# Performance work log

Measured on AMD Instinct MI355X. Metric: run time of the kernel, lower is better.

Reference implementation:

```python
import jax, jax.numpy as jnp
import numpy as np

DIM = 256
HEADS = 8
HD = DIM // HEADS          # 32
WS = 8                     # window size
TOPK = 4
SCALE = HD ** -0.5


def setup_inputs() -> dict:
    key = jax.random.key(0)
    k1, k2, k3 = jax.random.split(key, 3)
    B, H, W = 8, 64, 64
    x = jax.random.normal(k1, (B, DIM, H, W), dtype=jnp.float32)
    # 1x1 conv weights (BN folded -> weight + bias), fan-in scaled to keep logits sane
    w_qkv = jax.random.normal(k2, (3 * DIM, DIM), dtype=jnp.float32) / np.sqrt(DIM)
    b_qkv = jnp.zeros((3 * DIM,), dtype=jnp.float32)
    w_proj = jax.random.normal(k3, (DIM, DIM), dtype=jnp.float32) / np.sqrt(DIM)
    b_proj = jnp.zeros((DIM,), dtype=jnp.float32)
    return {"x": x, "w_qkv": w_qkv, "b_qkv": b_qkv, "w_proj": w_proj, "b_proj": b_proj}


def _window_partition(t, ws):
    # t: [BH, D, H, W] -> [BH, R, ws*ws, D]
    bh, d, h, w = t.shape
    gh, gw = h // ws, w // ws
    t = t.reshape(bh, d, gh, ws, gw, ws)
    t = t.transpose(0, 2, 4, 3, 5, 1)          # [BH, gh, gw, ws, ws, D]
    return t.reshape(bh, gh * gw, ws * ws, d)


def reference(x, w_qkv, b_qkv, w_proj, b_proj):
    B, C, H, W = x.shape
    gh, gw = H // WS, W // WS
    R, T = gh * gw, WS * WS
    BH = B * HEADS

    # qkv 1x1 conv
    qkv = jnp.einsum('bchw,oc->bohw', x, w_qkv) + b_qkv[None, :, None, None]
    q, k, v = jnp.split(qkv, 3, axis=1)                       # each [B, C, H, W]

    def to_bh(t):
        return t.reshape(BH, HD, H, W)

    q_w = _window_partition(to_bh(q), WS)                     # [BH, R, T, HD]
    k_w = _window_partition(to_bh(k), WS)
    v_w = _window_partition(to_bh(v), WS)

    # region-level routing: mean-pooled region tokens
    q_r = q_w.mean(axis=2)                                    # [BH, R, HD]
    k_r = k_w.mean(axis=2)
    attn_r = jnp.einsum('brd,bkd->brk', q_r, k_r) * SCALE     # [BH, R, R]
    topk = min(TOPK, R)
    _, topk_idx = jax.lax.top_k(attn_r, topk)                 # [BH, R, K]

    # gather top-k key/value windows per query region
    bidx = jnp.arange(BH)[:, None, None]
    k_sel = k_w[bidx, topk_idx]                               # [BH, R, K, T, HD]
    v_sel = v_w[bidx, topk_idx]
    k_sel = k_sel.reshape(BH, R, topk * T, HD)
    v_sel = v_sel.reshape(BH, R, topk * T, HD)

    # token-level attention inside routed regions
    attn = jnp.einsum('brtd,brsd->brts', q_w, k_sel) * SCALE  # [BH, R, T, K*T]
    attn = jax.nn.softmax(attn, axis=-1)
    out_w = jnp.einsum('brts,brsd->brtd', attn, v_sel)        # [BH, R, T, HD]

    # window reverse -> [BH, HD, H, W]
    out = out_w.reshape(BH, gh, gw, WS, WS, HD)
    out = out.transpose(0, 5, 1, 3, 2, 4).reshape(BH, HD, H, W)
    out = out.reshape(B, C, H, W)

    out = jnp.einsum('bchw,oc->bohw', out, w_proj) + b_proj[None, :, None, None]
    return out
```

## Files before the change

### kernel.cpp

```cpp
#include <hip/hip_runtime.h>
#include <hip/hip_bf16.h>

#define ATT_SCALE 0.17677669529663687f
#define EXP_C1 0.2550349235534668f
#define EXP_C2 23.083120654223400f

typedef short v8s __attribute__((ext_vector_type(8)));
typedef float v4f __attribute__((ext_vector_type(4)));
typedef float v16f __attribute__((ext_vector_type(16)));
typedef const __attribute__((address_space(1))) unsigned int gu32;
typedef __attribute__((address_space(3))) unsigned int lu32;

__device__ __forceinline__ void g2l16(const void* g, void* l) {
  __builtin_amdgcn_global_load_lds((gu32*)g, (lu32*)l, 16, 0, 0);
}

__device__ __forceinline__ float bflo(unsigned u){ union{unsigned i;float f;}x; x.i=u<<16; return x.f; }
__device__ __forceinline__ float bfhi(unsigned u){ union{unsigned i;float f;}x; x.i=u&0xffff0000u; return x.f; }
__device__ __forceinline__ unsigned short bf16r(float v){
  __hip_bfloat16 h = __float2bfloat16(v);
  return *reinterpret_cast<unsigned short*>(&h);
}
__device__ __forceinline__ unsigned pack_bf2(float a, float b){
  return (unsigned)bf16r(a) | ((unsigned)bf16r(b) << 16);
}
__device__ __forceinline__ unsigned cvtpk(float lo, float hi){
  unsigned r;
  asm("v_cvt_pk_bf16_f32 %0, %1, %2" : "=v"(r) : "v"(lo), "v"(hi));
  return r;
}
__device__ __forceinline__ void pl32swap(unsigned &a, unsigned &b){
  asm volatile("v_permlane32_swap_b32 %0, %1" : "+v"(a), "+v"(b));
}

__global__ __launch_bounds__(256) void k_prep(const float* __restrict__ x,
                                              const float* __restrict__ w_qkv,
                                              const float* __restrict__ w_proj,
                                              unsigned short* __restrict__ Xb,
                                              unsigned short* __restrict__ Wq,
                                              unsigned short* __restrict__ Wp,
                                              float* __restrict__ part) {
  __shared__ __align__(16) char hbuf[8192];
  __shared__ float pbuf[512];
  const int blk = blockIdx.x;
  const int t = threadIdx.x;
  if (blk >= 2048) {
    const int m = blk - 2048;
    const float* src = (m < 768) ? (w_qkv + m*256) : (w_proj + (size_t)(m - 768)*256);
    unsigned short* dst = (m < 768) ? (Wq + m*256) : (Wp + (size_t)(m - 768)*256);
    dst[t] = bf16r(src[t]);
    return;
  }
  const int b = blk >> 8, cc = (blk >> 6) & 3, pc = blk & 63;
  const int c0 = cc << 6, p0 = pc << 6;
  const int wv = t >> 6, lane = t & 63;

  float hi[16];
  const float* xp = x + ((size_t)(b*256 + c0 + wv*16))*4096 + p0 + lane;
  #pragma unroll
  for (int i = 0; i < 16; ++i) hi[i] = xp[(size_t)i*4096];

  #pragma unroll
  for (int i = 0; i < 16; ++i) {
    float s = hi[i];
    s += __shfl_xor(s, 1);
    s += __shfl_xor(s, 2);
    s += __shfl_xor(s, 4);
    if ((lane & 7) == 0) pbuf[(wv*16 + i)*8 + (lane >> 3)] = s;
  }

  #pragma unroll
  for (int gi = 0; gi < 2; ++gi) {
    uint4 uh;
    uh.x = pack_bf2(hi[gi*8+0], hi[gi*8+1]); uh.y = pack_bf2(hi[gi*8+2], hi[gi*8+3]);
    uh.z = pack_bf2(hi[gi*8+4], hi[gi*8+5]); uh.w = pack_bf2(hi[gi*8+6], hi[gi*8+7]);
    int off = lane*128 + ((wv*32 + gi*16) ^ ((lane & 7) << 4));
    *(uint4*)(hbuf + off) = uh;
  }
  __syncthreads();
  const size_t rowbase = ((size_t)(b*4096 + p0)) * 512 + (size_t)c0*2;
  #pragma unroll
  for (int s = 0; s < 2; ++s) {
    int gidx = s*256 + t;
    int row = gidx >> 3, gb = (gidx & 7) << 4;
    uint4 vh = *(const uint4*)(hbuf + row*128 + gb);
    *(uint4*)((char*)Xb + rowbase + (size_t)row*512 + gb) = vh;
  }
  const size_t pbase = ((size_t)(b*64 + pc)*256 + c0)*8;
  part[pbase + t]       = pbuf[t];
  part[pbase + 256 + t] = pbuf[t + 256];
}

__global__ __launch_bounds__(256) void k_xmr(const float* __restrict__ part,
                                             float* __restrict__ xmean) {
  const int blk = blockIdx.x;
  const int item = blk & 7;
  const int b = blk >> 6, rh = (blk >> 3) & 7;
  const int t = threadIdx.x;
  const int flat = item*256 + t;
  float acc = 0.f;
  const float* pp = part + (size_t)(b*64 + rh*8)*2048 + flat;
  #pragma unroll
  for (int j = 0; j < 8; ++j) acc += pp[(size_t)j*2048];
  const int c = flat >> 3, wc = flat & 7;
  xmean[(size_t)((b*256 + c) << 6) + (rh << 3) + wc] = acc * 0.015625f;
}

__global__ __launch_bounds__(256) void k_route(const float* __restrict__ xmean,
                                               const float* __restrict__ w_qkv,
                                               const float* __restrict__ b_qkv,
                                               int* __restrict__ topk) {
  __shared__ float xm[128][64];
  __shared__ float qr[64][33];
  __shared__ float kr[64][33];
  const int bh = blockIdx.x, b = bh >> 3, head = bh & 7;
  const int tid = threadIdx.x;
  const int d = tid & 31, r0 = tid >> 5;
  float qacc[8], kacc[8];
  const float bq = b_qkv[head*32 + d], bk = b_qkv[256 + head*32 + d];
  #pragma unroll
  for (int i = 0; i < 8; ++i) { qacc[i] = bq; kacc[i] = bk; }

  for (int c0 = 0; c0 < 256; c0 += 128) {
    __syncthreads();
    #pragma unroll
    for (int i = 0; i < 32; ++i) {
      int idx = i*256 + tid;
      int row = idx >> 6, col = idx & 63;
      xm[row][col] = xmean[(size_t)(b*256 + c0 + row)*64 + col];
    }
    __syncthreads();
    const float* wqp = w_qkv + (head*32 + d)*256 + c0;
    const float* wkp = w_qkv + (256 + head*32 + d)*256 + c0;
    for (int c = 0; c < 128; ++c) {
      float wq = wqp[c], wk = wkp[c];
      #pragma unroll
      for (int i = 0; i < 8; ++i) {
        float xv = xm[c][r0 + 8*i];
        qacc[i] += wq * xv;
        kacc[i] += wk * xv;
      }
    }
  }
  #pragma unroll
  for (int i = 0; i < 8; ++i) { qr[r0+8*i][d] = qacc[i]; kr[r0+8*i][d] = kacc[i]; }
  __syncthreads();

  float* ar = &xm[0][0];
  for (int item = tid; item < 4096; item += 256) {
    int i = item >> 6, j = item & 63;
    float s = 0.f;
    #pragma unroll
    for (int dd = 0; dd < 32; ++dd) s += qr[i][dd]*kr[j][dd];
    ar[i*64 + j] = s;
  }
  __syncthreads();
  if (tid < 64) {
    for (int kk = 0; kk < 4; ++kk) {
      float best = -3e38f; int bj = 0;
      for (int j = 0; j < 64; ++j) {
        float v = ar[tid*64 + j];
        if (v > best) { best = v; bj = j; }
      }
      ar[tid*64 + bj] = -3e38f;
      topk[(bh*64 + tid)*4 + kk] = bj;
    }
  }
}

template<int EPI>
__global__ __launch_bounds__(256) void k_gemm(
    const unsigned short* __restrict__ Wstk,
    const unsigned short* __restrict__ Bmat,
    const float* __restrict__ bias,
    unsigned short* __restrict__ qbuf, unsigned short* __restrict__ kbuf,
    unsigned short* __restrict__ vbuf, float* __restrict__ outp) {
  __shared__ __align__(16) char lds[32768];
  const int tid = threadIdx.x;
  const int wv = tid >> 6, lane = tid & 63;
  const int nt = blockIdx.x, mt = blockIdx.y;

  const char* xsrc = (const char*)Bmat
      + (size_t)(nt*64 + (lane >> 5))*512 + (lane & 31)*16;
  #pragma unroll
  for (int o = 0; o < 8; ++o) {
    int op = wv*8 + o;
    g2l16(xsrc + (size_t)(op*2)*512, lds + op*1024);
  }

  const char* wrowbase = (const char*)Wstk
      + ((size_t)(mt*128 + wv*32 + (lane & 15)))*512 + ((lane >> 4) << 4);
  v8s a[4][2][2];
  #pragma unroll
  for (int kt = 0; kt < 4; ++kt)
    #pragma unroll
    for (int kk = 0; kk < 2; ++kk)
      #pragma unroll
      for (int i = 0; i < 2; ++i)
        a[kt][kk][i] = *(const v8s*)(wrowbase + (size_t)(i*16)*512 + kt*128 + kk*64);

  v4f acc[2][4];
  #pragma unroll
  for (int i = 0; i < 2; ++i)
    #pragma unroll
    for (int j = 0; j < 4; ++j) acc[i][j] = (v4f){0.f,0.f,0.f,0.f};

  asm volatile("s_waitcnt vmcnt(0)" ::: "memory");
  __syncthreads();

  #pragma unroll
  for (int kt = 0; kt < 4; ++kt) {
    #pragma unroll
    for (int kk = 0; kk < 2; ++kk) {
      const int kb = kk*64 + ((lane>>4)<<4);
      v8s b[4];
      #pragma unroll
      for (int j = 0; j < 4; ++j) {
        int nr = j*16 + (lane & 15);
        b[j] = *(const v8s*)(lds + nr*512 + kt*128 + (kb ^ ((nr & 7) << 4)));
      }
      #pragma unroll
      for (int i = 0; i < 2; ++i)
        #pragma unroll
        for (int j = 0; j < 4; ++j)
          acc[i][j] = __builtin_amdgcn_mfma_f32_16x16x32_bf16(a[kt][kk][i], b[j], acc[i][j], 0, 0, 0);
    }
  }

  if (EPI == 0) {
    if (mt < 4) {
      unsigned short* outbuf = (mt < 2) ? qbuf : kbuf;
      #pragma unroll
      for (int i = 0; i < 2; ++i) {
        int o = mt*128 + wv*32 + i*16 + ((lane >> 4) << 2);
        int head = (o >> 5) & 7, d0 = o & 31;
        float b0 = bias[o], b1 = bias[o+1], b2 = bias[o+2], b3 = bias[o+3];
        #pragma unroll
        for (int j = 0; j < 4; ++j) {
          int p = nt*64 + j*16 + (lane & 15);
          int bb = p >> 12, ploc = p & 4095;
          int h = ploc >> 6, w = ploc & 63;
          int rr = ((h >> 3) << 3) | (w >> 3), tt = ((h & 7) << 3) | (w & 7);
          int bh = bb*8 + head;
          uint2 u;
          u.x = pack_bf2(acc[i][j][0] + b0, acc[i][j][1] + b1);
          u.y = pack_bf2(acc[i][j][2] + b2, acc[i][j][3] + b3);
          *(uint2*)(outbuf + (size_t)(((bh << 6) | rr)*64 + tt)*32 + d0) = u;
        }
      }
    } else {
      #pragma unroll
      for (int i = 0; i < 2; ++i) {
        int o = mt*128 + wv*32 + i*16 + ((lane >> 4) << 2);
        int vch = o - 512;
        int head = vch >> 5, d0 = vch & 31;
        float bv[4] = {bias[o], bias[o+1], bias[o+2], bias[o+3]};
        #pragma unroll
        for (int j = 0; j < 4; ++j) {
          int p = nt*64 + j*16 + (lane & 15);
          int bb = p >> 12, ploc = p & 4095;
          int h = ploc >> 6, w = ploc & 63;
          int rr = ((h >> 3) << 3) | (w >> 3), tt = ((h & 7) << 3) | (w & 7);
          int bh = bb*8 + head;
          size_t base = ((size_t)((bh << 6) | rr)*32 + d0)*64 + tt;
          #pragma unroll
          for (int c = 0; c < 4; ++c)
            vbuf[base + (size_t)c*64] = bf16r(acc[i][j][c] + bv[c]);
        }
      }
    }
  } else {
    #pragma unroll
    for (int i = 0; i < 2; ++i) {
      int o = mt*128 + wv*32 + i*16 + ((lane >> 4) << 2);
      float b0 = bias[o], b1 = bias[o+1], b2 = bias[o+2], b3 = bias[o+3];
      #pragma unroll
      for (int j = 0; j < 4; ++j) {
        int p = nt*64 + j*16 + (lane & 15);
        int bb = p >> 12, ploc = p & 4095;
        float* dst = outp + ((size_t)(bb*256 + o))*4096 + ploc;
        dst[0]     = acc[i][j][0] + b0;
        dst[4096]  = acc[i][j][1] + b1;
        dst[8192]  = acc[i][j][2] + b2;
        dst[12288] = acc[i][j][3] + b3;
      }
    }
  }
}

__global__ __launch_bounds__(256) void k_attn(const unsigned short* __restrict__ qw,
                                              const unsigned short* __restrict__ kw,
                                              const unsigned short* __restrict__ vwt,
                                              const int* __restrict__ topk,
                                              unsigned short* __restrict__ owt) {
  const int lane = threadIdx.x & 63;
  const int W = blockIdx.x*4 + (threadIdx.x >> 6);
  const int bh = W >> 6, rr = W & 63;
  const int lo5 = lane & 31, hi = lane >> 5;
  const int b = bh >> 3, head = bh & 7;

  const unsigned short* qb = qw + (size_t)(bh*64 + rr)*2048;
  v8s qf[2][2];
  #pragma unroll
  for (int qt = 0; qt < 2; ++qt)
    #pragma unroll
    for (int ck = 0; ck < 2; ++ck)
      qf[qt][ck] = *(const v8s*)(qb + (qt*32 + lo5)*32 + ck*16 + hi*8);

  int idx4[4];
  #pragma unroll
  for (int w = 0; w < 4; ++w) idx4[w] = topk[(bh*64 + rr)*4 + w];

  v16f O[2];
  #pragma unroll
  for (int qt = 0; qt < 2; ++qt)
    #pragma unroll
    for (int r = 0; r < 16; ++r) O[qt][r] = 0.f;
  float lsum[2] = {0.f, 0.f};

  #pragma unroll
  for (int w = 0; w < 4; ++w) {
    const unsigned short* kb = kw  + (size_t)(bh*64 + idx4[w])*2048;
    const unsigned short* vb = vwt + (size_t)(bh*64 + idx4[w])*2048;
    v8s kf[2][2], vf[4];
    #pragma unroll
    for (int kt = 0; kt < 2; ++kt)
      #pragma unroll
      for (int ck = 0; ck < 2; ++ck)
        kf[kt][ck] = *(const v8s*)(kb + (kt*32 + lo5)*32 + ck*16 + hi*8);
    #pragma unroll
    for (int mk = 0; mk < 4; ++mk)
      vf[mk] = *(const v8s*)(vb + lo5*64 + mk*16 + hi*8);

    v16f S[2][2];
    #pragma unroll
    for (int kt = 0; kt < 2; ++kt)
      #pragma unroll
      for (int qt = 0; qt < 2; ++qt) {
        v16f z;
        #pragma unroll
        for (int r = 0; r < 16; ++r) z[r] = 0.f;
        z = __builtin_amdgcn_mfma_f32_32x32x16_bf16(kf[kt][0], qf[qt][0], z, 0, 0, 0);
        S[kt][qt] = __builtin_amdgcn_mfma_f32_32x32x16_bf16(kf[kt][1], qf[qt][1], z, 0, 0, 0);
      }

    #pragma unroll
    for (int kt = 0; kt < 2; ++kt) {
      #pragma unroll
      for (int qt = 0; qt < 2; ++qt) {
        float p[16];
        #pragma unroll
        for (int r = 0; r < 16; ++r)
          p[r] = __builtin_amdgcn_exp2f(__builtin_fmaf(S[kt][qt][r], EXP_C1, -EXP_C2));
        float s01 = (p[0]+p[1]) + (p[2]+p[3]);
        float s23 = (p[4]+p[5]) + (p[6]+p[7]);
        float s45 = (p[8]+p[9]) + (p[10]+p[11]);
        float s67 = (p[12]+p[13]) + (p[14]+p[15]);
        lsum[qt] += (s01 + s23) + (s45 + s67);

        unsigned wh[8], wl[8];
        #pragma unroll
        for (int i = 0; i < 8; ++i) {
          wh[i] = cvtpk(p[2*i], p[2*i+1]);
          float l0 = p[2*i]   - bflo(wh[i]);
          float l1 = p[2*i+1] - bfhi(wh[i]);
          wl[i] = cvtpk(l0, l1);
        }
        pl32swap(wh[0], wh[2]); pl32swap(wh[1], wh[3]);
        pl32swap(wh[4], wh[6]); pl32swap(wh[5], wh[7]);
        pl32swap(wl[0], wl[2]); pl32swap(wl[1], wl[3]);
        pl32swap(wl[4], wl[6]); pl32swap(wl[5], wl[7]);
        union { unsigned u[4]; v8s v; } fA, fB;
        fA.u[0] = wh[0]; fA.u[1] = wh[1]; fA.u[2] = wh[2]; fA.u[3] = wh[3];
        fB.u[0] = wl[0]; fB.u[1] = wl[1]; fB.u[2] = wl[2]; fB.u[3] = wl[3];
        O[qt] = __builtin_amdgcn_mfma_f32_32x32x16_bf16(fA.v, vf[2*kt], O[qt], 0, 0, 0);
        O[qt] = __builtin_amdgcn_mfma_f32_32x32x16_bf16(fB.v, vf[2*kt], O[qt], 0, 0, 0);
        fA.u[0] = wh[4]; fA.u[1] = wh[5]; fA.u[2] = wh[6]; fA.u[3] = wh[7];
        fB.u[0] = wl[4]; fB.u[1] = wl[5]; fB.u[2] = wl[6]; fB.u[3] = wl[7];
        O[qt] = __builtin_amdgcn_mfma_f32_32x32x16_bf16(fA.v, vf[2*kt+1], O[qt], 0, 0, 0);
        O[qt] = __builtin_amdgcn_mfma_f32_32x32x16_bf16(fB.v, vf[2*kt+1], O[qt], 0, 0, 0);
      }
    }
  }

  float linv[2];
  #pragma unroll
  for (int qt = 0; qt < 2; ++qt) {
    float t = lsum[qt] + __shfl_xor(lsum[qt], 32);
    linv[qt] = 1.0f / t;
  }

  #pragma unroll
  for (int qt = 0; qt < 2; ++qt) {
    #pragma unroll
    for (int r = 0; r < 16; ++r) {
      int q = (r & 3) + 8*(r >> 2) + 4*hi;
      float li = __shfl(linv[qt], q);
      float val = O[qt][r] * li;
      int tok = qt*32 + q;
      int h = ((rr >> 3) << 3) | (tok >> 3);
      int wcol = ((rr & 7) << 3) | (tok & 7);
      int pg = (b << 12) | (h << 6) | wcol;
      int col = ((head >> 1) << 6) | ((((head & 1) << 5) + lo5) ^ ((tok & 7) << 3));
      owt[(size_t)pg*256 + col] = bf16r(val);
    }
  }
}

extern "C" void kernel_launch(void* const* d_in, const int* in_sizes, int n_in,
                              void* d_out, int out_size, void* d_ws, size_t ws_size,
                              hipStream_t stream) {
  (void)in_sizes; (void)n_in; (void)out_size; (void)ws_size;
  const float* x      = (const float*)d_in[0];
  const float* w_qkv  = (const float*)d_in[1];
  const float* b_qkv  = (const float*)d_in[2];
  const float* w_proj = (const float*)d_in[3];
  const float* b_proj = (const float*)d_in[4];
  float* out = (float*)d_out;

  char* ws = (char*)d_ws;
  unsigned short* Xb  = (unsigned short*)ws;
  unsigned short* Wq  = (unsigned short*)(ws + 16777216);
  unsigned short* Wp  = (unsigned short*)(ws + 17170432);
  unsigned short* qw  = (unsigned short*)(ws + 17301504);
  unsigned short* kw  = (unsigned short*)(ws + 34078720);
  unsigned short* vwt = (unsigned short*)(ws + 50855936);
  float* part         = (float*)(ws + 67633152);
  float* xmean        = (float*)(ws + 71827456);
  int* topk           = (int*)(ws + 72351744);
  unsigned short* owt = Xb;

  k_prep <<<dim3(3072), 256, 0, stream>>>(x, w_qkv, w_proj, Xb, Wq, Wp, part);
  k_xmr  <<<dim3(512),  256, 0, stream>>>(part, xmean);
  k_route<<<dim3(64),   256, 0, stream>>>(xmean, w_qkv, b_qkv, topk);
  k_gemm<0><<<dim3(512, 6), 256, 0, stream>>>(Wq, Xb, b_qkv, qw, kw, vwt, nullptr);
  k_attn <<<dim3(1024), 256, 0, stream>>>(qw, kw, vwt, topk, owt);
  k_gemm<1><<<dim3(512, 2), 256, 0, stream>>>(Wp, owt, b_proj, nullptr, nullptr, nullptr, out);
}
```

Measured before the change: 129.9 us.

## Loop over M tiles inside GEMM block to reuse LDS activation tile

```diff
diff --git a/kernel.cpp b/kernel.cpp
--- a/kernel.cpp
+++ b/kernel.cpp
@@ -168,8 +168,8 @@
   }
 }
 
-template<int EPI>
-__global__ __launch_bounds__(256) void k_gemm(
+template<int MT, int EPI>
+__global__ __launch_bounds__(256, 2) void k_gemm(
     const unsigned short* __restrict__ Wstk,
     const unsigned short* __restrict__ Bmat,
     const float* __restrict__ bias,
@@ -178,7 +178,7 @@
   __shared__ __align__(16) char lds[32768];
   const int tid = threadIdx.x;
   const int wv = tid >> 6, lane = tid & 63;
-  const int nt = blockIdx.x, mt = blockIdx.y;
+  const int nt = blockIdx.x;
 
   const char* xsrc = (const char*)Bmat
       + (size_t)(nt*64 + (lane >> 5))*512 + (lane & 31)*16;
@@ -188,101 +188,115 @@
     g2l16(xsrc + (size_t)(op*2)*512, lds + op*1024);
   }
 
-  const char* wrowbase = (const char*)Wstk
-      + ((size_t)(mt*128 + wv*32 + (lane & 15)))*512 + ((lane >> 4) << 4);
-  v8s a[4][2][2];
-  #pragma unroll
-  for (int kt = 0; kt < 4; ++kt)
-    #pragma unroll
-    for (int kk = 0; kk < 2; ++kk)
-      #pragma unroll
-      for (int i = 0; i < 2; ++i)
-        a[kt][kk][i] = *(const v8s*)(wrowbase + (size_t)(i*16)*512 + kt*128 + kk*64);
-
-  v4f acc[2][4];
+  const char* wbase = (const char*)Wstk
+      + ((size_t)(wv*32 + (lane & 15)))*512 + ((lane >> 4) << 4);
+  v8s wbuf[2][16];
   #pragma unroll
   for (int i = 0; i < 2; ++i)
     #pragma unroll
-    for (int j = 0; j < 4; ++j) acc[i][j] = (v4f){0.f,0.f,0.f,0.f};
+    for (int kt = 0; kt < 4; ++kt)
+      #pragma unroll
+      for (int kk = 0; kk < 2; ++kk)
+        wbuf[0][i*8+kt*2+kk] = *(const v8s*)(wbase + (size_t)(i*16)*512 + kt*128 + kk*64);
 
   asm volatile("s_waitcnt vmcnt(0)" ::: "memory");
   __syncthreads();
 
   #pragma unroll
-  for (int kt = 0; kt < 4; ++kt) {
-    #pragma unroll
-    for (int kk = 0; kk < 2; ++kk) {
-      const int kb = kk*64 + ((lane>>4)<<4);
-      v8s b[4];
-      #pragma unroll
-      for (int j = 0; j < 4; ++j) {
-        int nr = j*16 + (lane & 15);
-        b[j] = *(const v8s*)(lds + nr*512 + kt*128 + (kb ^ ((nr & 7) << 4)));
-      }
+  for (int m = 0; m < MT; ++m) {
+    if (m + 1 < MT) {
+      const char* wb2 = wbase + (size_t)((m+1)*128)*512;
       #pragma unroll
       for (int i = 0; i < 2; ++i)
         #pragma unroll
-        for (int j = 0; j < 4; ++j)
-          acc[i][j] = __builtin_amdgcn_mfma_f32_16x16x32_bf16(a[kt][kk][i], b[j], acc[i][j], 0, 0, 0);
-    }
-  }
-
-  if (EPI == 0) {
-    if (mt < 4) {
-      unsigned short* outbuf = (mt < 2) ? qbuf : kbuf;
+        for (int kt = 0; kt < 4; ++kt)
+          #pragma unroll
+          for (int kk = 0; kk < 2; ++kk)
+            wbuf[(m+1)&1][i*8+kt*2+kk] = *(const v8s*)(wb2 + (size_t)(i*16)*512 + kt*128 + kk*64);
+    }
+
+    v4f acc[2][4];
+    #pragma unroll
+    for (int i = 0; i < 2; ++i)
+      #pragma unroll
+      for (int j = 0; j < 4; ++j) acc[i][j] = (v4f){0.f,0.f,0.f,0.f};
+
+    #pragma unroll
+    for (int kt = 0; kt < 4; ++kt) {
+      #pragma unroll
+      for (int kk = 0; kk < 2; ++kk) {
+        const int kb = kk*64 + ((lane>>4)<<4);
+        v8s b[4];
+        #pragma unroll
+        for (int j = 0; j < 4; ++j) {
+          int nr = j*16 + (lane & 15);
+          b[j] = *(const v8s*)(lds + nr*512 + kt*128 + (kb ^ ((nr & 7) << 4)));
+        }
+        #pragma unroll
+        for (int i = 0; i < 2; ++i)
+          #pragma unroll
+          for (int j = 0; j < 4; ++j)
+            acc[i][j] = __builtin_amdgcn_mfma_f32_16x16x32_bf16(wbuf[m&1][i*8+kt*2+kk], b[j], acc[i][j], 0, 0, 0);
+      }
+    }
+
+    if (EPI == 0) {
+      if (m < 4) {
+        unsigned short* outbuf = (m < 2) ? qbuf : kbuf;
+        #pragma unroll
+        for (int i = 0; i < 2; ++i) {
+          int o = m*128 + wv*32 + i*16 + ((lane >> 4) << 2);
+          int head = (o >> 5) & 7, d0 = o & 31;
+          float b0 = bias[o], b1 = bias[o+1], b2 = bias[o+2], b3 = bias[o+3];
+          #pragma unroll
+          for (int j = 0; j < 4; ++j) {
+            int p = nt*64 + j*16 + (lane & 15);
+            int bb = p >> 12, ploc = p & 4095;
+            int h = ploc >> 6, w = ploc & 63;
+            int rr = ((h >> 3) << 3) | (w >> 3), tt = ((h & 7) << 3) | (w & 7);
+            int bh = bb*8 + head;
+            uint2 u;
+            u.x = pack_bf2(acc[i][j][0] + b0, acc[i][j][1] + b1);
+            u.y = pack_bf2(acc[i][j][2] + b2, acc[i][j][3] + b3);
+            *(uint2*)(outbuf + (size_t)(((bh << 6) | rr)*64 + tt)*32 + d0) = u;
+          }
+        }
+      } else {
+        #pragma unroll
+        for (int i = 0; i < 2; ++i) {
+          int o = m*128 + wv*32 + i*16 + ((lane >> 4) << 2);
+          int vch = o - 512;
+          int head = vch >> 5, d0 = vch & 31;
+          float bv[4] = {bias[o], bias[o+1], bias[o+2], bias[o+3]};
+          #pragma unroll
+          for (int j = 0; j < 4; ++j) {
+            int p = nt*64 + j*16 + (lane & 15);
+            int bb = p >> 12, ploc = p & 4095;
+            int h = ploc >> 6, w = ploc & 63;
+            int rr = ((h >> 3) << 3) | (w >> 3), tt = ((h & 7) << 3) | (w & 7);
+            int bh = bb*8 + head;
+            size_t base = ((size_t)((bh << 6) | rr)*32 + d0)*64 + tt;
+            #pragma unroll
+            for (int c = 0; c < 4; ++c)
+              vbuf[base + (size_t)c*64] = bf16r(acc[i][j][c] + bv[c]);
+          }
+        }
+      }
+    } else {
       #pragma unroll
       for (int i = 0; i < 2; ++i) {
-        int o = mt*128 + wv*32 + i*16 + ((lane >> 4) << 2);
-        int head = (o >> 5) & 7, d0 = o & 31;
+        int o = m*128 + wv*32 + i*16 + ((lane >> 4) << 2);
         float b0 = bias[o], b1 = bias[o+1], b2 = bias[o+2], b3 = bias[o+3];
         #pragma unroll
         for (int j = 0; j < 4; ++j) {
           int p = nt*64 + j*16 + (lane & 15);
           int bb = p >> 12, ploc = p & 4095;
-          int h = ploc >> 6, w = ploc & 63;
-          int rr = ((h >> 3) << 3) | (w >> 3), tt = ((h & 7) << 3) | (w & 7);
-          int bh = bb*8 + head;
-          uint2 u;
-          u.x = pack_bf2(acc[i][j][0] + b0, acc[i][j][1] + b1);
-          u.y = pack_bf2(acc[i][j][2] + b2, acc[i][j][3] + b3);
-          *(uint2*)(outbuf + (size_t)(((bh << 6) | rr)*64 + tt)*32 + d0) = u;
+          float* dst = outp + ((size_t)(bb*256 + o))*4096 + ploc;
+          dst[0]     = acc[i][j][0] + b0;
+          dst[4096]  = acc[i][j][1] + b1;
+          dst[8192]  = acc[i][j][2] + b2;
+          dst[12288] = acc[i][j][3] + b3;
         }
-      }
-    } else {
-      #pragma unroll
-      for (int i = 0; i < 2; ++i) {
-        int o = mt*128 + wv*32 + i*16 + ((lane >> 4) << 2);
-        int vch = o - 512;
-        int head = vch >> 5, d0 = vch & 31;
-        float bv[4] = {bias[o], bias[o+1], bias[o+2], bias[o+3]};
-        #pragma unroll
-        for (int j = 0; j < 4; ++j) {
-          int p = nt*64 + j*16 + (lane & 15);
-          int bb = p >> 12, ploc = p & 4095;
-          int h = ploc >> 6, w = ploc & 63;
-          int rr = ((h >> 3) << 3) | (w >> 3), tt = ((h & 7) << 3) | (w & 7);
-          int bh = bb*8 + head;
-          size_t base = ((size_t)((bh << 6) | rr)*32 + d0)*64 + tt;
-          #pragma unroll
-          for (int c = 0; c < 4; ++c)
-            vbuf[base + (size_t)c*64] = bf16r(acc[i][j][c] + bv[c]);
-        }
-      }
-    }
-  } else {
-    #pragma unroll
-    for (int i = 0; i < 2; ++i) {
-      int o = mt*128 + wv*32 + i*16 + ((lane >> 4) << 2);
-      float b0 = bias[o], b1 = bias[o+1], b2 = bias[o+2], b3 = bias[o+3];
-      #pragma unroll
-      for (int j = 0; j < 4; ++j) {
-        int p = nt*64 + j*16 + (lane & 15);
-        int bb = p >> 12, ploc = p & 4095;
-        float* dst = outp + ((size_t)(bb*256 + o))*4096 + ploc;
-        dst[0]     = acc[i][j][0] + b0;
-        dst[4096]  = acc[i][j][1] + b1;
-        dst[8192]  = acc[i][j][2] + b2;
-        dst[12288] = acc[i][j][3] + b3;
       }
     }
   }
@@ -433,7 +447,7 @@
   k_prep <<<dim3(3072), 256, 0, stream>>>(x, w_qkv, w_proj, Xb, Wq, Wp, part);
   k_xmr  <<<dim3(512),  256, 0, stream>>>(part, xmean);
   k_route<<<dim3(64),   256, 0, stream>>>(xmean, w_qkv, b_qkv, topk);
-  k_gemm<0><<<dim3(512, 6), 256, 0, stream>>>(Wq, Xb, b_qkv, qw, kw, vwt, nullptr);
+  k_gemm<6,0><<<dim3(512), 256, 0, stream>>>(Wq, Xb, b_qkv, qw, kw, vwt, nullptr);
   k_attn <<<dim3(1024), 256, 0, stream>>>(qw, kw, vwt, topk, owt);
-  k_gemm<1><<<dim3(512, 2), 256, 0, stream>>>(Wp, owt, b_proj, nullptr, nullptr, nullptr, out);
-}
+  k_gemm<2,1><<<dim3(512), 256, 0, stream>>>(Wp, owt, b_proj, nullptr, nullptr, nullptr, out);
+}
```

Result: faster. 126.9 us (-2.3%).

## Enlarge GEMM M-tile to 256 and stage swizzled weights through LDS per K-step

Applied to the files above, without the earlier changes.

```diff
diff --git a/kernel.cpp b/kernel.cpp
--- a/kernel.cpp
+++ b/kernel.cpp
@@ -48,7 +48,8 @@
     const int m = blk - 2048;
     const float* src = (m < 768) ? (w_qkv + m*256) : (w_proj + (size_t)(m - 768)*256);
     unsigned short* dst = (m < 768) ? (Wq + m*256) : (Wp + (size_t)(m - 768)*256);
-    dst[t] = bf16r(src[t]);
+    int col = (t & ~63) | ((t & 63) ^ ((m & 7) << 3));
+    dst[col] = bf16r(src[t]);
     return;
   }
   const int b = blk >> 8, cc = (blk >> 6) & 3, pc = blk & 63;
@@ -175,64 +176,62 @@
     const float* __restrict__ bias,
     unsigned short* __restrict__ qbuf, unsigned short* __restrict__ kbuf,
     unsigned short* __restrict__ vbuf, float* __restrict__ outp) {
-  __shared__ __align__(16) char lds[32768];
+  __shared__ __align__(16) char lds[40960];
   const int tid = threadIdx.x;
   const int wv = tid >> 6, lane = tid & 63;
   const int nt = blockIdx.x, mt = blockIdx.y;
 
-  const char* xsrc = (const char*)Bmat
-      + (size_t)(nt*64 + (lane >> 5))*512 + (lane & 31)*16;
-  #pragma unroll
-  for (int o = 0; o < 8; ++o) {
-    int op = wv*8 + o;
-    g2l16(xsrc + (size_t)(op*2)*512, lds + op*1024);
-  }
-
-  const char* wrowbase = (const char*)Wstk
-      + ((size_t)(mt*128 + wv*32 + (lane & 15)))*512 + ((lane >> 4) << 4);
-  v8s a[4][2][2];
-  #pragma unroll
-  for (int kt = 0; kt < 4; ++kt)
-    #pragma unroll
-    for (int kk = 0; kk < 2; ++kk)
-      #pragma unroll
-      for (int i = 0; i < 2; ++i)
-        a[kt][kk][i] = *(const v8s*)(wrowbase + (size_t)(i*16)*512 + kt*128 + kk*64);
-
-  v4f acc[2][4];
-  #pragma unroll
-  for (int i = 0; i < 2; ++i)
+  v4f acc[4][4];
+  #pragma unroll
+  for (int i = 0; i < 4; ++i)
     #pragma unroll
     for (int j = 0; j < 4; ++j) acc[i][j] = (v4f){0.f,0.f,0.f,0.f};
 
-  asm volatile("s_waitcnt vmcnt(0)" ::: "memory");
-  __syncthreads();
-
-  #pragma unroll
+  const char* wlanebase = (const char*)Wstk + ((size_t)(mt*256) + (lane>>3))*512 + (lane&7)*16;
+  const size_t prowlane = (size_t)(nt*64 + (lane>>3))*512 + (lane&7)*16;
+
   for (int kt = 0; kt < 4; ++kt) {
+    const int k0b = kt * 128;
+    __syncthreads();
+    #pragma unroll
+    for (int o = 0; o < 8; ++o) {
+      int op = wv*8 + o;
+      g2l16(wlanebase + (size_t)(op*8)*512 + k0b, lds + op*1024);
+    }
+    #pragma unroll
+    for (int o = 0; o < 2; ++o) {
+      int op = wv*2 + o;
+      g2l16((const char*)Bmat + prowlane + (size_t)(op*8)*512 + k0b, lds + 32768 + op*1024);
+    }
+    __syncthreads();
     #pragma unroll
     for (int kk = 0; kk < 2; ++kk) {
       const int kb = kk*64 + ((lane>>4)<<4);
-      v8s b[4];
+      v8s a[4], b[4];
+      #pragma unroll
+      for (int i = 0; i < 4; ++i) {
+        int mr = wv*64 + i*16 + (lane & 15);
+        a[i] = *(const v8s*)(lds + mr*128 + (kb ^ ((mr & 7) << 4)));
+      }
       #pragma unroll
       for (int j = 0; j < 4; ++j) {
         int nr = j*16 + (lane & 15);
-        b[j] = *(const v8s*)(lds + nr*512 + kt*128 + (kb ^ ((nr & 7) << 4)));
-      }
-      #pragma unroll
-      for (int i = 0; i < 2; ++i)
+        b[j] = *(const v8s*)(lds + 32768 + nr*128 + (kb ^ ((nr & 7) << 4)));
+      }
+      #pragma unroll
+      for (int i = 0; i < 4; ++i)
         #pragma unroll
         for (int j = 0; j < 4; ++j)
-          acc[i][j] = __builtin_amdgcn_mfma_f32_16x16x32_bf16(a[kt][kk][i], b[j], acc[i][j], 0, 0, 0);
+          acc[i][j] = __builtin_amdgcn_mfma_f32_16x16x32_bf16(a[i], b[j], acc[i][j], 0, 0, 0);
     }
   }
 
   if (EPI == 0) {
-    if (mt < 4) {
-      unsigned short* outbuf = (mt < 2) ? qbuf : kbuf;
-      #pragma unroll
-      for (int i = 0; i < 2; ++i) {
-        int o = mt*128 + wv*32 + i*16 + ((lane >> 4) << 2);
+    if (mt < 2) {
+      unsigned short* outbuf = (mt == 0) ? qbuf : kbuf;
+      #pragma unroll
+      for (int i = 0; i < 4; ++i) {
+        int o = mt*256 + wv*64 + i*16 + ((lane >> 4) << 2);
         int head = (o >> 5) & 7, d0 = o & 31;
         float b0 = bias[o], b1 = bias[o+1], b2 = bias[o+2], b3 = bias[o+3];
         #pragma unroll
@@ -250,8 +249,8 @@
       }
     } else {
       #pragma unroll
-      for (int i = 0; i < 2; ++i) {
-        int o = mt*128 + wv*32 + i*16 + ((lane >> 4) << 2);
+      for (int i = 0; i < 4; ++i) {
+        int o = 512 + wv*64 + i*16 + ((lane >> 4) << 2);
         int vch = o - 512;
         int head = vch >> 5, d0 = vch & 31;
         float bv[4] = {bias[o], bias[o+1], bias[o+2], bias[o+3]};
@@ -271,8 +270,8 @@
     }
   } else {
     #pragma unroll
-    for (int i = 0; i < 2; ++i) {
-      int o = mt*128 + wv*32 + i*16 + ((lane >> 4) << 2);
+    for (int i = 0; i < 4; ++i) {
+      int o = wv*64 + i*16 + ((lane >> 4) << 2);
       float b0 = bias[o], b1 = bias[o+1], b2 = bias[o+2], b3 = bias[o+3];
       #pragma unroll
       for (int j = 0; j < 4; ++j) {
@@ -433,7 +432,7 @@
   k_prep <<<dim3(3072), 256, 0, stream>>>(x, w_qkv, w_proj, Xb, Wq, Wp, part);
   k_xmr  <<<dim3(512),  256, 0, stream>>>(part, xmean);
   k_route<<<dim3(64),   256, 0, stream>>>(xmean, w_qkv, b_qkv, topk);
-  k_gemm<0><<<dim3(512, 6), 256, 0, stream>>>(Wq, Xb, b_qkv, qw, kw, vwt, nullptr);
+  k_gemm<0><<<dim3(512, 3), 256, 0, stream>>>(Wq, Xb, b_qkv, qw, kw, vwt, nullptr);
   k_attn <<<dim3(1024), 256, 0, stream>>>(qw, kw, vwt, topk, owt);
-  k_gemm<1><<<dim3(512, 2), 256, 0, stream>>>(Wp, owt, b_proj, nullptr, nullptr, nullptr, out);
-}
+  k_gemm<1><<<dim3(512, 1), 256, 0, stream>>>(Wp, owt, b_proj, nullptr, nullptr, nullptr, out);
+}
```

After: 119.0 us. 1.09x faster.
